# Kernel tuning notes

Measured on AMD Instinct MI355X. Metric: run time of the kernel, lower is better.

## Reference

```python
import jax, jax.numpy as jnp
import numpy as np

D_MODEL = 1024
NUM_HEADS = 16
D_K = D_MODEL // NUM_HEADS


def setup_inputs() -> dict:
    key = jax.random.key(0)
    ks = jax.random.split(key, 11)
    B, S = 2, 2048
    s = 1.0 / np.sqrt(D_MODEL)
    return {
        "q": jax.random.normal(ks[0], (B, S, D_MODEL), jnp.float32),
        "k": jax.random.normal(ks[1], (B, S, D_MODEL), jnp.float32),
        "v": jax.random.normal(ks[2], (B, S, D_MODEL), jnp.float32),
        "w_q": jax.random.normal(ks[3], (D_MODEL, D_MODEL), jnp.float32) * s,
        "b_q": jnp.zeros((D_MODEL,), jnp.float32),
        "w_k": jax.random.normal(ks[4], (D_MODEL, D_MODEL), jnp.float32) * s,
        "b_k": jnp.zeros((D_MODEL,), jnp.float32),
        "w_v": jax.random.normal(ks[5], (D_MODEL, D_MODEL), jnp.float32) * s,
        "b_v": jnp.zeros((D_MODEL,), jnp.float32),
        "w_o": jax.random.normal(ks[6], (D_MODEL, D_MODEL), jnp.float32) * s,
        "b_o": jnp.zeros((D_MODEL,), jnp.float32),
    }


def reference(q, k, v, w_q, b_q, w_k, b_k, w_v, b_v, w_o, b_o):
    B, S, _ = q.shape
    H, Dk = NUM_HEADS, D_K

    def split_heads(x):  # [B,S,D] -> [B,H,S,Dk]
        return x.reshape(B, S, H, Dk).transpose(0, 2, 1, 3)

    # torch nn.Linear: x @ W.T + b
    qh = split_heads(q @ w_q.T + b_q)
    kh = split_heads(k @ w_k.T + b_k)
    vh = split_heads(v @ w_v.T + b_v)

    scale = 1.0 / jnp.sqrt(jnp.asarray(Dk, qh.dtype))
    scores = jnp.einsum("bhsd,bhtd->bhst", qh, kh) * scale  # [B,H,S,S]
    attn = jax.nn.softmax(scores, axis=-1)
    # dropout is identity in eval/deterministic baseline
    out = jnp.einsum("bhst,bhtd->bhsd", attn, vh)  # [B,H,S,Dk]
    out = out.transpose(0, 2, 1, 3).reshape(B, S, H * Dk)
    return out @ w_o.T + b_o
```

## Files before the change

### kernel.cpp

```cpp
#include <hip/hip_runtime.h>
#include <hip/hip_bf16.h>
#include <stdint.h>

typedef unsigned short u16;
typedef __attribute__((ext_vector_type(8))) short short8;
typedef __attribute__((ext_vector_type(8))) __bf16 bf16x8;
typedef __attribute__((ext_vector_type(4))) float f32x4;
typedef __attribute__((ext_vector_type(4))) uint32_t u32x4;

#if defined(__has_builtin)
#if __has_builtin(__builtin_amdgcn_global_load_lds)
#define USE_GLLDS 1
#endif
#endif

#if defined(__has_builtin)
#if __has_builtin(__builtin_amdgcn_exp2f)
#define HAVE_EXP2_BUILTIN 1
#endif
#endif
__device__ __forceinline__ float fexp2(float x) {
#ifdef HAVE_EXP2_BUILTIN
  return __builtin_amdgcn_exp2f(x);
#else
  return exp2f(x);
#endif
}

__device__ __forceinline__ u16 f2bf(float f) {
  __hip_bfloat16 h = __float2bfloat16(f);
  return __builtin_bit_cast(u16, h);
}

__device__ __forceinline__ uint32_t cvt_pk_bf16(float lo, float hi) {
  uint32_t w;
  asm("v_cvt_pk_bf16_f32 %0, %1, %2" : "=v"(w) : "v"(lo), "v"(hi));
  return w;
}

__device__ __forceinline__ short8 pack8_f32(const float* p) {
  const float4 lo = *(const float4*)p;
  const float4 hi = *(const float4*)(p + 4);
  union { uint32_t u[4]; short8 s; } r;
  r.u[0] = cvt_pk_bf16(lo.x, lo.y);
  r.u[1] = cvt_pk_bf16(lo.z, lo.w);
  r.u[2] = cvt_pk_bf16(hi.x, hi.y);
  r.u[3] = cvt_pk_bf16(hi.z, hi.w);
  return r.s;
}

__device__ __forceinline__ f32x4 mfma16(bf16x8 a, bf16x8 b, f32x4 c) {
  return __builtin_amdgcn_mfma_f32_16x16x32_bf16(a, b, c, 0, 0, 0);
}

#ifdef USE_GLLDS
__device__ __forceinline__ void async_cp16(const void* g, void* l) {
  __builtin_amdgcn_global_load_lds(
      (const __attribute__((address_space(1))) void*)g,
      (__attribute__((address_space(3))) void*)l, 16, 0, 0);
}
#endif

template <int A_F32, int B_F32>
__device__ __forceinline__ void gemm_core8(const void* __restrict__ Xv,
                                           const void* __restrict__ Wv,
                                           const float* __restrict__ bias,
                                           void* __restrict__ outp, int mode,
                                           int m0, int n0) {
  __shared__ u16 Al[128 * 64];
  __shared__ u16 Bl[128 * 64];
  const int tid = threadIdx.x;
  const int wv = tid >> 6, l = tid & 63;
  const int wr = wv >> 2, wc = wv & 3;
  const int lrow = l & 15, g = l >> 4;
  const int rswe = (lrow & 7) << 3;

  f32x4 acc[4][2];
#pragma unroll
  for (int i = 0; i < 4; ++i)
#pragma unroll
    for (int j = 0; j < 2; ++j) acc[i][j] = (f32x4){0.f, 0.f, 0.f, 0.f};

  const int srow = l >> 3;
  const int ccol = l & 7;
  const int gchunk = ccol ^ srow;
  const int arow = wv * 8 + srow;

  for (int kt = 0; kt < 1024; kt += 64) {
    if (A_F32) {
      const float* Af = (const float*)Xv;
      const float* pa = Af + (size_t)(m0 + arow) * 1024 + kt + gchunk * 8;
      short8 a0 = pack8_f32(pa);
      short8 a1 = pack8_f32(pa + (size_t)64 * 1024);
      *(short8*)&Al[arow * 64 + ccol * 8] = a0;
      *(short8*)&Al[(arow + 64) * 64 + ccol * 8] = a1;
    } else {
      const u16* Ab = (const u16*)Xv;
      const u16* Asrc = Ab + (size_t)(m0 + arow) * 1024 + kt + gchunk * 8;
#ifdef USE_GLLDS
      async_cp16(Asrc, &Al[(wv * 8) * 64]);
      async_cp16(Asrc + (size_t)64 * 1024, &Al[(wv * 8 + 64) * 64]);
#else
      short8 a0 = *(const short8*)Asrc;
      short8 a1 = *(const short8*)(Asrc + (size_t)64 * 1024);
      *(short8*)&Al[arow * 64 + ccol * 8] = a0;
      *(short8*)&Al[(arow + 64) * 64 + ccol * 8] = a1;
#endif
    }
    if (B_F32) {
      const float* Wf = (const float*)Wv;
      const float* pb = Wf + (size_t)arow * 1024 + kt + gchunk * 8;
      short8 b0 = pack8_f32(pb);
      short8 b1 = pack8_f32(pb + (size_t)64 * 1024);
      *(short8*)&Bl[arow * 64 + ccol * 8] = b0;
      *(short8*)&Bl[(arow + 64) * 64 + ccol * 8] = b1;
    } else {
      const u16* Wb = (const u16*)Wv;
      const u16* Bsrc = Wb + (size_t)arow * 1024 + kt + gchunk * 8;
#ifdef USE_GLLDS
      async_cp16(Bsrc, &Bl[(wv * 8) * 64]);
      async_cp16(Bsrc + (size_t)64 * 1024, &Bl[(wv * 8 + 64) * 64]);
#else
      short8 b0 = *(const short8*)Bsrc;
      short8 b1 = *(const short8*)(Bsrc + (size_t)64 * 1024);
      *(short8*)&Bl[arow * 64 + ccol * 8] = b0;
      *(short8*)&Bl[(arow + 64) * 64 + ccol * 8] = b1;
#endif
    }
    __syncthreads();
#pragma unroll
    for (int ks = 0; ks < 2; ++ks) {
      bf16x8 af[4], bf[2];
      const int qoff = (((ks * 4 + g) << 3) ^ rswe);
#pragma unroll
      for (int mf = 0; mf < 4; ++mf)
        af[mf] = *(const bf16x8*)&Al[(wr * 64 + mf * 16 + lrow) * 64 + qoff];
#pragma unroll
      for (int nf = 0; nf < 2; ++nf)
        bf[nf] = *(const bf16x8*)&Bl[(wc * 32 + nf * 16 + lrow) * 64 + qoff];
      __builtin_amdgcn_s_setprio(1);
#pragma unroll
      for (int mf = 0; mf < 4; ++mf)
#pragma unroll
        for (int nf = 0; nf < 2; ++nf)
          acc[mf][nf] = mfma16(af[mf], bf[nf], acc[mf][nf]);
      __builtin_amdgcn_s_setprio(0);
    }
    __syncthreads();
  }

  const int rb = (l >> 4) * 4;
#pragma unroll
  for (int mf = 0; mf < 4; ++mf) {
#pragma unroll
    for (int nf = 0; nf < 2; ++nf) {
      const int gn = n0 + wc * 32 + nf * 16 + lrow;
      const float bi = bias[gn];
#pragma unroll
      for (int r = 0; r < 4; ++r) {
        const int gm = m0 + wr * 64 + mf * 16 + rb + r;
        float val = acc[mf][nf][r] + bi;
        const int b = gm >> 11, s = gm & 2047, h = gn >> 6, d = gn & 63;
        if (mode == 3) {
          ((float*)outp)[(size_t)gm * 1024 + gn] = val;
        } else if (mode == 2) {
          ((u16*)outp)[(((size_t)((b * 16 + h) * 64 + d)) << 11) + s] = f2bf(val);
        } else {
          if (mode == 0) val *= 0.18033688f;
          ((u16*)outp)[(((size_t)((b * 16 + h) * 2048 + s)) << 6) + d] = f2bf(val);
        }
      }
    }
  }
}

__global__ __launch_bounds__(512, 6) void gemm_proj(
    const float* __restrict__ q, const float* __restrict__ k,
    const float* __restrict__ v, const float* __restrict__ w_q,
    const float* __restrict__ w_k, const float* __restrict__ w_v,
    const float* __restrict__ b_q, const float* __restrict__ b_k,
    const float* __restrict__ b_v, u16* __restrict__ Qh) {
  const int s = blockIdx.x;
  const int xcd = s & 7, c = s >> 3;
  const int nx = (xcd >> 2) * 12 + (c % 12);
  const int my = (xcd & 3) * 8 + (c / 12);
  const int z = nx >> 3, nxl = nx & 7;
  const float* X = (z == 0) ? q : ((z == 1) ? k : v);
  const float* W = (z == 0) ? w_q : ((z == 1) ? w_k : w_v);
  const float* bias = (z == 0) ? b_q : ((z == 1) ? b_k : b_v);
  gemm_core8<1, 1>(X, W + ((size_t)nxl << 17), bias, Qh + ((size_t)z << 22),
                   z, my * 128, nxl * 128);
}

__global__ __launch_bounds__(512, 6) void gemm_out(
    const u16* __restrict__ X, const float* __restrict__ W,
    const float* __restrict__ bias, float* __restrict__ out) {
  const int s = blockIdx.x;
  const int xcd = s & 7, c = s >> 3;
  const int nx = (xcd >> 2) * 4 + (c & 3);
  const int my = (xcd & 3) * 8 + (c >> 2);
  gemm_core8<0, 1>(X, W + ((size_t)nx << 17), bias, out, 3, my * 128,
                   nx * 128);
}

__global__ __launch_bounds__(512, 4) void flash_attn8(
    const u16* __restrict__ Qh, const u16* __restrict__ Kh,
    const u16* __restrict__ VT, u16* __restrict__ Op,
    float2* __restrict__ ml) {
  __shared__ __align__(16) u16 Kbuf[2][4096];
  __shared__ __align__(16) u16 Vbuf[2][4096];
  __shared__ __align__(16) uint32_t Pl[8 * 576];

  const int tid = threadIdx.x;
  const int wv = tid >> 6, l = tid & 63;
  const int q = l & 15, g = l >> 4;

  const int s_lin = blockIdx.x + (blockIdx.y << 4) + (blockIdx.z << 9);
  const int o = ((s_lin & 7) << 7) + (s_lin >> 3);
  const int qt = o & 15, bh = (o >> 4) & 31, z = o >> 9;

  const u16* Qp = Qh + ((size_t)bh * 2048 + qt * 128 + wv * 16) * 64;
  const u16* Kp = Kh + (size_t)bh * 2048 * 64;
  const u16* Vp = VT + (size_t)bh * 64 * 2048;

  bf16x8 qf[2];
  qf[0] = *(const bf16x8*)(Qp + q * 64 + g * 8);
  qf[1] = *(const bf16x8*)(Qp + q * 64 + 32 + g * 8);

  f32x4 o_acc[4];
#pragma unroll
  for (int df = 0; df < 4; ++df) o_acc[df] = (f32x4){0.f, 0.f, 0.f, 0.f};
  float m = -1e30f, ls = 0.f;

  const int srow = l >> 3;
  const int scolq = (l & 7) ^ srow;
  const int pbase = wv * 576 + q * 36;
  const char* kb0 = (const char*)&Kbuf[0][0];
  const char* kb1 = (const char*)&Kbuf[1][0];
  const char* vb0 = (const char*)&Vbuf[0][0];
  const char* vb1 = (const char*)&Vbuf[1][0];
  const int rsw = (q & 7) << 4;

  const u16* kg = Kp + (size_t)(z * 1024 + wv * 8 + srow) * 64 + scolq * 8;
  const u16* vg = Vp + (size_t)(wv * 8 + srow) * 2048 + z * 1024 + scolq * 8;

  {
    short8 k0 = *(const short8*)kg;
    short8 k1 = *(const short8*)(kg + 4096);
    short8 v0 = *(const short8*)vg;
    short8 v1 = *(const short8*)(vg + 64);
    *(short8*)&Kbuf[0][wv * 512 + l * 8] = k0;
    *(short8*)&Kbuf[1][wv * 512 + l * 8] = k1;
    *(short8*)&Vbuf[0][wv * 512 + l * 8] = v0;
    *(short8*)&Vbuf[1][wv * 512 + l * 8] = v1;
  }
  kg += 8192;
  vg += 128;
  __syncthreads();

  for (int tt = 0; tt < 8; ++tt) {
    short8 kr0, kr1, vr0, vr1;
    if (tt < 7) {
      kr0 = *(const short8*)kg;
      kr1 = *(const short8*)(kg + 4096);
      vr0 = *(const short8*)vg;
      vr1 = *(const short8*)(vg + 64);
      kg += 8192;
      vg += 128;
    }

    f32x4 s0[4], s1[4];
#pragma unroll
    for (int nj = 0; nj < 4; ++nj) {
      s0[nj] = (f32x4){0.f, 0.f, 0.f, 0.f};
      s1[nj] = (f32x4){0.f, 0.f, 0.f, 0.f};
    }
    __builtin_amdgcn_s_setprio(1);
#pragma unroll
    for (int ks = 0; ks < 2; ++ks) {
#pragma unroll
      for (int nj = 0; nj < 4; ++nj) {
        const int off = (nj * 16 + q) * 128 + (((ks * 4 + g) << 4) ^ rsw);
        bf16x8 kf0 = *(const bf16x8*)(kb0 + off);
        bf16x8 kf1 = *(const bf16x8*)(kb1 + off);
        s0[nj] = mfma16(kf0, qf[ks], s0[nj]);
        s1[nj] = mfma16(kf1, qf[ks], s1[nj]);
      }
    }
    __builtin_amdgcn_s_setprio(0);

    float mt = s0[0][0];
#pragma unroll
    for (int nj = 0; nj < 4; ++nj)
#pragma unroll
      for (int r = 0; r < 4; ++r) {
        mt = fmaxf(mt, s0[nj][r]);
        mt = fmaxf(mt, s1[nj][r]);
      }
    mt = fmaxf(mt, __shfl_xor(mt, 16));
    mt = fmaxf(mt, __shfl_xor(mt, 32));
    if (!__all(mt <= m + 8.f)) {
      const float nm = fmaxf(m, mt);
      const float rf = fexp2(m - nm);
      m = nm;
      ls *= rf;
#pragma unroll
      for (int df = 0; df < 4; ++df) o_acc[df] *= rf;
    }
    float ps = 0.f;
#pragma unroll
    for (int nj = 0; nj < 4; ++nj)
#pragma unroll
      for (int r = 0; r < 4; ++r) {
        s0[nj][r] = fexp2(s0[nj][r] - m);
        s1[nj][r] = fexp2(s1[nj][r] - m);
        ps += s0[nj][r] + s1[nj][r];
      }
    ps += __shfl_xor(ps, 16);
    ps += __shfl_xor(ps, 32);
    ls += ps;

#pragma unroll
    for (int nj = 0; nj < 4; ++nj)
#pragma unroll
      for (int pp = 0; pp < 2; ++pp)
        Pl[pbase + nj * 8 + g * 2 + pp] =
            cvt_pk_bf16(s0[nj][2 * pp], s0[nj][2 * pp + 1]);
    __builtin_amdgcn_s_setprio(1);
#pragma unroll
    for (int ks = 0; ks < 2; ++ks) {
      u32x4 pw = *(const u32x4*)&Pl[pbase + ks * 16 + 4 * g];
      bf16x8 pf = __builtin_bit_cast(bf16x8, pw);
#pragma unroll
      for (int df = 0; df < 4; ++df) {
        bf16x8 vf = *(const bf16x8*)(vb0 + (df * 16 + q) * 128 +
                                     (((ks * 4 + g) << 4) ^ rsw));
        o_acc[df] = mfma16(vf, pf, o_acc[df]);
      }
    }
    __builtin_amdgcn_s_setprio(0);

#pragma unroll
    for (int nj = 0; nj < 4; ++nj)
#pragma unroll
      for (int pp = 0; pp < 2; ++pp)
        Pl[pbase + nj * 8 + g * 2 + pp] =
            cvt_pk_bf16(s1[nj][2 * pp], s1[nj][2 * pp + 1]);
    __builtin_amdgcn_s_setprio(1);
#pragma unroll
    for (int ks = 0; ks < 2; ++ks) {
      u32x4 pw = *(const u32x4*)&Pl[pbase + ks * 16 + 4 * g];
      bf16x8 pf = __builtin_bit_cast(bf16x8, pw);
#pragma unroll
      for (int df = 0; df < 4; ++df) {
        bf16x8 vf = *(const bf16x8*)(vb1 + (df * 16 + q) * 128 +
                                     (((ks * 4 + g) << 4) ^ rsw));
        o_acc[df] = mfma16(vf, pf, o_acc[df]);
      }
    }
    __builtin_amdgcn_s_setprio(0);

    __syncthreads();
    if (tt < 7) {
      *(short8*)&Kbuf[0][wv * 512 + l * 8] = kr0;
      *(short8*)&Kbuf[1][wv * 512 + l * 8] = kr1;
      *(short8*)&Vbuf[0][wv * 512 + l * 8] = vr0;
      *(short8*)&Vbuf[1][wv * 512 + l * 8] = vr1;
    }
    __syncthreads();
  }

  const float inv = 1.f / ls;
  const int rowb = qt * 128 + wv * 16 + q;
  const size_t prow = (size_t)(z * 32 + bh) * 2048 + rowb;
  u16* Po = Op + (prow << 6);
#pragma unroll
  for (int df = 0; df < 4; ++df)
#pragma unroll
    for (int pp = 0; pp < 2; ++pp) {
      uint32_t w = cvt_pk_bf16(o_acc[df][2 * pp] * inv,
                               o_acc[df][2 * pp + 1] * inv);
      *(uint32_t*)(Po + df * 16 + 4 * g + 2 * pp) = w;
    }
  if (g == 0) ml[prow] = make_float2(m, ls);
}

__global__ __launch_bounds__(256) void combine(
    const uint32_t* __restrict__ Op32, const float2* __restrict__ ml,
    u16* __restrict__ AO) {
  const int j = blockIdx.x * 256 + threadIdx.x;
  const int rowid = j >> 5, w5 = j & 31;
  const float2 a = ml[rowid];
  const float2 c = ml[(1 << 16) + rowid];
  const float M = fmaxf(a.x, c.x);
  float w1 = a.y * fexp2(a.x - M);
  float w2 = c.y * fexp2(c.x - M);
  const float inv = 1.f / (w1 + w2);
  w1 *= inv;
  w2 *= inv;
  const uint32_t p1 = Op32[j];
  const uint32_t p2 = Op32[(1u << 21) + j];
  const float lo = w1 * __builtin_bit_cast(float, p1 << 16) +
                   w2 * __builtin_bit_cast(float, p2 << 16);
  const float hi = w1 * __builtin_bit_cast(float, p1 & 0xffff0000u) +
                   w2 * __builtin_bit_cast(float, p2 & 0xffff0000u);
  const uint32_t outw = cvt_pk_bf16(lo, hi);
  const int bh = rowid >> 11, s = rowid & 2047, b = bh >> 4, h = bh & 15;
  ((uint32_t*)AO)[((size_t)(b * 2048 + s) << 9) + h * 32 + w5] = outw;
}

extern "C" void kernel_launch(void* const* d_in, const int* in_sizes, int n_in,
                              void* d_out, int out_size, void* d_ws,
                              size_t ws_size, hipStream_t stream) {
  const float* q = (const float*)d_in[0];
  const float* k = (const float*)d_in[1];
  const float* v = (const float*)d_in[2];
  const float* w_q = (const float*)d_in[3];
  const float* b_q = (const float*)d_in[4];
  const float* w_k = (const float*)d_in[5];
  const float* b_k = (const float*)d_in[6];
  const float* w_v = (const float*)d_in[7];
  const float* b_v = (const float*)d_in[8];
  const float* w_o = (const float*)d_in[9];
  const float* b_o = (const float*)d_in[10];

  u16* ws = (u16*)d_ws;
  u16* Qh = ws + (16u << 20);
  u16* Kh = ws + (20u << 20);
  u16* VT = ws + (24u << 20);
  u16* AO = ws + (28u << 20);
  u16* Op = ws;
  float2* ml = (float2*)(ws + (8u << 20));

  gemm_proj<<<dim3(768), dim3(512), 0, stream>>>(q, k, v, w_q, w_k, w_v, b_q,
                                                 b_k, b_v, Qh);
  flash_attn8<<<dim3(16, 32, 2), dim3(512), 0, stream>>>(Qh, Kh, VT, Op, ml);
  combine<<<dim3(8192), dim3(256), 0, stream>>>((const uint32_t*)Op, ml, AO);
  gemm_out<<<dim3(256), dim3(512), 0, stream>>>(AO, w_o, b_o, (float*)d_out);
}
```

Baseline: 142.0 us.

## Prefetch next GEMM K-tile into registers while computing current tile

Restructures the GEMM main loop into a register-prefetch software pipeline. Global loads for the next 64-wide K slice are issued before the MFMA work on the current slice and written to LDS (with bf16 conversion) after a barrier, so load latency overlaps compute. The unused global_load_lds path is removed. Launch bounds drop from 6 to 4 waves-per-EU hints to give room for the extra prefetch registers, which may lower occupancy and adds a second barrier per iteration.

After: 145.4 us. +2.4%, slower.

```diff
diff --git a/kernel.cpp b/kernel.cpp
--- a/kernel.cpp
+++ b/kernel.cpp
@@ -7,12 +7,6 @@
 typedef __attribute__((ext_vector_type(8))) __bf16 bf16x8;
 typedef __attribute__((ext_vector_type(4))) float f32x4;
 typedef __attribute__((ext_vector_type(4))) uint32_t u32x4;
-
-#if defined(__has_builtin)
-#if __has_builtin(__builtin_amdgcn_global_load_lds)
-#define USE_GLLDS 1
-#endif
-#endif
 
 #if defined(__has_builtin)
 #if __has_builtin(__builtin_amdgcn_exp2f)
@@ -38,9 +32,7 @@
   return w;
 }
 
-__device__ __forceinline__ short8 pack8_f32(const float* p) {
-  const float4 lo = *(const float4*)p;
-  const float4 hi = *(const float4*)(p + 4);
+__device__ __forceinline__ short8 pack8_reg(float4 lo, float4 hi) {
   union { uint32_t u[4]; short8 s; } r;
   r.u[0] = cvt_pk_bf16(lo.x, lo.y);
   r.u[1] = cvt_pk_bf16(lo.z, lo.w);
@@ -52,14 +44,6 @@
 __device__ __forceinline__ f32x4 mfma16(bf16x8 a, bf16x8 b, f32x4 c) {
   return __builtin_amdgcn_mfma_f32_16x16x32_bf16(a, b, c, 0, 0, 0);
 }
-
-#ifdef USE_GLLDS
-__device__ __forceinline__ void async_cp16(const void* g, void* l) {
-  __builtin_amdgcn_global_load_lds(
-      (const __attribute__((address_space(1))) void*)g,
-      (__attribute__((address_space(3))) void*)l, 16, 0, 0);
-}
-#endif
 
 template <int A_F32, int B_F32>
 __device__ __forceinline__ void gemm_core8(const void* __restrict__ Xv,
@@ -86,48 +70,58 @@
   const int gchunk = ccol ^ srow;
   const int arow = wv * 8 + srow;
 
+  const float* Af = (const float*)Xv;
+  const u16* Ab = (const u16*)Xv;
+  const float* Wf = (const float*)Wv;
+  const u16* Wb = (const u16*)Wv;
+  const size_t aoff = (size_t)(m0 + arow) * 1024 + gchunk * 8;
+  const size_t boff = (size_t)arow * 1024 + gchunk * 8;
+
+  float4 la0, la1, la2, la3, lb0, lb1, lb2, lb3;
+  short8 sa0, sa1, sb0, sb1;
+
+#define GLOAD(kt)                                                             \
+  do {                                                                        \
+    if (A_F32) {                                                              \
+      const float* pa = Af + aoff + (kt);                                     \
+      la0 = *(const float4*)pa;                                               \
+      la1 = *(const float4*)(pa + 4);                                         \
+      la2 = *(const float4*)(pa + (size_t)64 * 1024);                         \
+      la3 = *(const float4*)(pa + (size_t)64 * 1024 + 4);                     \
+    } else {                                                                  \
+      const u16* pa = Ab + aoff + (kt);                                       \
+      sa0 = *(const short8*)pa;                                               \
+      sa1 = *(const short8*)(pa + (size_t)64 * 1024);                         \
+    }                                                                         \
+    if (B_F32) {                                                              \
+      const float* pb = Wf + boff + (kt);                                     \
+      lb0 = *(const float4*)pb;                                               \
+      lb1 = *(const float4*)(pb + 4);                                         \
+      lb2 = *(const float4*)(pb + (size_t)64 * 1024);                         \
+      lb3 = *(const float4*)(pb + (size_t)64 * 1024 + 4);                     \
+    } else {                                                                  \
+      const u16* pb = Wb + boff + (kt);                                       \
+      sb0 = *(const short8*)pb;                                               \
+      sb1 = *(const short8*)(pb + (size_t)64 * 1024);                         \
+    }                                                                         \
+  } while (0)
+
+#define LWRITE()                                                              \
+  do {                                                                        \
+    if (A_F32) { sa0 = pack8_reg(la0, la1); sa1 = pack8_reg(la2, la3); }      \
+    if (B_F32) { sb0 = pack8_reg(lb0, lb1); sb1 = pack8_reg(lb2, lb3); }      \
+    *(short8*)&Al[arow * 64 + ccol * 8] = sa0;                                \
+    *(short8*)&Al[(arow + 64) * 64 + ccol * 8] = sa1;                         \
+    *(short8*)&Bl[arow * 64 + ccol * 8] = sb0;                                \
+    *(short8*)&Bl[(arow + 64) * 64 + ccol * 8] = sb1;                         \
+  } while (0)
+
+  GLOAD(0);
+  LWRITE();
+  __syncthreads();
+
   for (int kt = 0; kt < 1024; kt += 64) {
-    if (A_F32) {
-      const float* Af = (const float*)Xv;
-      const float* pa = Af + (size_t)(m0 + arow) * 1024 + kt + gchunk * 8;
-      short8 a0 = pack8_f32(pa);
-      short8 a1 = pack8_f32(pa + (size_t)64 * 1024);
-      *(short8*)&Al[arow * 64 + ccol * 8] = a0;
-      *(short8*)&Al[(arow + 64) * 64 + ccol * 8] = a1;
-    } else {
-      const u16* Ab = (const u16*)Xv;
-      const u16* Asrc = Ab + (size_t)(m0 + arow) * 1024 + kt + gchunk * 8;
-#ifdef USE_GLLDS
-      async_cp16(Asrc, &Al[(wv * 8) * 64]);
-      async_cp16(Asrc + (size_t)64 * 1024, &Al[(wv * 8 + 64) * 64]);
-#else
-      short8 a0 = *(const short8*)Asrc;
-      short8 a1 = *(const short8*)(Asrc + (size_t)64 * 1024);
-      *(short8*)&Al[arow * 64 + ccol * 8] = a0;
-      *(short8*)&Al[(arow + 64) * 64 + ccol * 8] = a1;
-#endif
-    }
-    if (B_F32) {
-      const float* Wf = (const float*)Wv;
-      const float* pb = Wf + (size_t)arow * 1024 + kt + gchunk * 8;
-      short8 b0 = pack8_f32(pb);
-      short8 b1 = pack8_f32(pb + (size_t)64 * 1024);
-      *(short8*)&Bl[arow * 64 + ccol * 8] = b0;
-      *(short8*)&Bl[(arow + 64) * 64 + ccol * 8] = b1;
-    } else {
-      const u16* Wb = (const u16*)Wv;
-      const u16* Bsrc = Wb + (size_t)arow * 1024 + kt + gchunk * 8;
-#ifdef USE_GLLDS
-      async_cp16(Bsrc, &Bl[(wv * 8) * 64]);
-      async_cp16(Bsrc + (size_t)64 * 1024, &Bl[(wv * 8 + 64) * 64]);
-#else
-      short8 b0 = *(const short8*)Bsrc;
-      short8 b1 = *(const short8*)(Bsrc + (size_t)64 * 1024);
-      *(short8*)&Bl[arow * 64 + ccol * 8] = b0;
-      *(short8*)&Bl[(arow + 64) * 64 + ccol * 8] = b1;
-#endif
-    }
-    __syncthreads();
+    if (kt < 960) GLOAD(kt + 64);
 #pragma unroll
     for (int ks = 0; ks < 2; ++ks) {
       bf16x8 af[4], bf[2];
@@ -147,7 +141,11 @@
       __builtin_amdgcn_s_setprio(0);
     }
     __syncthreads();
+    if (kt < 960) LWRITE();
+    __syncthreads();
   }
+#undef GLOAD
+#undef LWRITE
 
   const int rb = (l >> 4) * 4;
 #pragma unroll
@@ -174,7 +172,7 @@
   }
 }
 
-__global__ __launch_bounds__(512, 6) void gemm_proj(
+__global__ __launch_bounds__(512, 4) void gemm_proj(
     const float* __restrict__ q, const float* __restrict__ k,
     const float* __restrict__ v, const float* __restrict__ w_q,
     const float* __restrict__ w_k, const float* __restrict__ w_v,
@@ -192,7 +190,7 @@
                    z, my * 128, nxl * 128);
 }
 
-__global__ __launch_bounds__(512, 6) void gemm_out(
+__global__ __launch_bounds__(512, 4) void gemm_out(
     const u16* __restrict__ X, const float* __restrict__ W,
     const float* __restrict__ bias, float* __restrict__ out) {
   const int s = blockIdx.x;
```
